# Optimization experiments

Measured on AMD Instinct MI355X. Metric: run time of the kernel, lower is better.

## Reference

```python
import jax, jax.numpy as jnp
import numpy as np

B, N, D = 1, 768, 256
H = 4
HD = D // H
K = 16
EDGE_DIM = 4
LN_EPS = 1e-5


def setup_inputs() -> dict:
    key = jax.random.key(0)
    ks = jax.random.split(key, 16)
    g = lambda k, shape, fan: jax.random.normal(k, shape, jnp.float32) / np.sqrt(fan)
    return {
        'x': jax.random.normal(ks[0], (B, N, D), jnp.float32),
        'Wqkv_w': g(ks[1], (D, 3 * D), D), 'Wqkv_b': jnp.zeros((3 * D,), jnp.float32),
        'out_w': g(ks[2], (D, D), D), 'out_b': jnp.zeros((D,), jnp.float32),
        'ffn1_w': g(ks[3], (2 * D, 2 * D), 2 * D), 'ffn1_b': jnp.zeros((2 * D,), jnp.float32),
        'ln_g': jnp.ones((2 * D,), jnp.float32), 'ln_b': jnp.zeros((2 * D,), jnp.float32),
        'ffn2_w': g(ks[4], (2 * D, D), 2 * D), 'ffn2_b': jnp.zeros((D,), jnp.float32),
        'e1_w': g(ks[5], (EDGE_DIM, 2 * H), EDGE_DIM), 'e1_b': jnp.zeros((2 * H,), jnp.float32),
        'e2_w': g(ks[6], (2 * H, H), 2 * H), 'e2_b': jnp.zeros((H,), jnp.float32),
        'graph_gate': jnp.float32(0.5),
    }


def _normalize(v):
    return v / jnp.clip(jnp.linalg.norm(v, axis=-1, keepdims=True), 1e-12)


def reference(x, Wqkv_w, Wqkv_b, out_w, out_b, ffn1_w, ffn1_b, ln_g, ln_b,
              ffn2_w, ffn2_b, e1_w, e1_b, e2_w, e2_b, graph_gate):
    b, n, d = x.shape
    # ---- graph topology (no grad, discrete top-k) ----
    xs = jax.lax.stop_gradient(x)
    dn_s = _normalize(xs)
    sim_d = jnp.einsum('bnd,bmd->bnm', dn_s, dn_s)
    eye = jnp.eye(n, dtype=bool)
    sim_d = jnp.where(eye, -jnp.inf, sim_d)
    idx = jax.lax.top_k(sim_d, K)[1]                       # (B,N,K)
    adj = jnp.zeros((b, n, n), bool).at[
        jnp.arange(b)[:, None, None], jnp.arange(n)[None, :, None], idx].set(True)
    adj = adj | jnp.swapaxes(adj, 1, 2) | eye              # symmetric + self loops
    # ---- differentiable edge features (B,N,N,4) ----
    dnm = _normalize(x)
    sim = jnp.einsum('bnd,bmd->bnm', dnm, dnm)
    diff = x[:, :, None, :] - x[:, None, :, :]             # (B,N,N,D) memory-bound
    l2 = jnp.linalg.norm(diff, axis=-1) / np.float32(np.sqrt(d))
    ad = jnp.abs(diff)
    ef = jnp.stack([sim, l2, ad.mean(-1), ad.max(-1)], axis=-1)
    # ---- edge bias per head (B,H,N,N) ----
    h = jax.nn.relu(ef @ e1_w + e1_b)
    bias = jnp.transpose(h @ e2_w + e2_b, (0, 3, 1, 2))
    # ---- attention ----
    qkv = (x @ Wqkv_w + Wqkv_b).reshape(b, n, H, HD, 3)
    qkv = jnp.transpose(qkv, (0, 2, 1, 3, 4))              # (B,H,N,HD,3)
    q, k, v = qkv[..., 0], qkv[..., 1], qkv[..., 2]
    logits = jnp.einsum('bhnd,bhmd->bhnm', q, k) / np.float32(np.sqrt(HD))
    logits = logits + graph_gate * bias
    logits = jnp.where(adj[:, None], logits, -jnp.inf)     # sparse masking
    attn = jax.nn.softmax(logits, axis=-1)
    ctx = jnp.einsum('bhnm,bhmd->bhnd', attn, v)
    msg = jnp.transpose(ctx, (0, 2, 1, 3)).reshape(b, n, d) @ out_w + out_b
    # ---- FFN: Linear -> LayerNorm -> GELU -> Linear, residual ----
    y = jnp.concatenate([x, msg], axis=-1) @ ffn1_w + ffn1_b
    mu = y.mean(-1, keepdims=True)
    var = ((y - mu) ** 2).mean(-1, keepdims=True)
    y = (y - mu) / jnp.sqrt(var + LN_EPS) * ln_g + ln_b
    y = jax.nn.gelu(y, approximate=False)
    return x + (y @ ffn2_w + ffn2_b)
```

## Files before the change

### kernel.cpp

```cpp
#include <hip/hip_runtime.h>
#include <hip/hip_bf16.h>
#include <math.h>

#define NN 768
#define DD 256
#define NHEAD 4
#define HDIM 64
#define TOPK 16

typedef __attribute__((ext_vector_type(8))) short short8;
typedef __attribute__((ext_vector_type(4))) float f32x4;

__device__ __forceinline__ unsigned short f2bf(float f) {
    unsigned u = __float_as_uint(f);
    unsigned r = u + 0x7fffu + ((u >> 16) & 1u);
    return (unsigned short)(r >> 16);
}

__global__ __launch_bounds__(64) void k_norms(const float* __restrict__ x,
                                              double* __restrict__ nrm2_d,
                                              double* __restrict__ nrm_d,
                                              double* __restrict__ invn_d,
                                              unsigned short* __restrict__ xb,
                                              unsigned int* __restrict__ adjw) {
    int n = blockIdx.x;
    int lane = threadIdx.x;
    int gid = n * 64 + lane;
    adjw[gid * 3 + 0] = 0u;
    adjw[gid * 3 + 1] = 0u;
    adjw[gid * 3 + 2] = 0u;
    const float* row = x + (size_t)n * DD;
    double s = 0.0;
    #pragma unroll
    for (int i = 0; i < 4; ++i) {
        float v = row[lane + 64 * i];
        xb[(size_t)n * DD + lane + 64 * i] = f2bf(v);
        s += (double)v * (double)v;
    }
    for (int off = 32; off > 0; off >>= 1) s += __shfl_down(s, off);
    if (lane == 0) {
        nrm2_d[n] = s;
        double nv = sqrt(s);
        nrm_d[n] = nv;
        invn_d[n] = 1.0 / fmax(nv, 1e-12);
    }
}

__global__ __launch_bounds__(256) void k_prep(const float* __restrict__ Wqkv,
                                              const float* __restrict__ outw,
                                              const float* __restrict__ f1w,
                                              const float* __restrict__ f2w,
                                              unsigned short* __restrict__ t_qkv,
                                              unsigned short* __restrict__ t_out,
                                              unsigned short* __restrict__ t_f1,
                                              unsigned short* __restrict__ t_f2) {
    int b = blockIdx.x;
    const float* src; unsigned short* dst; int K, C, tile;
    if (b < 192)      { src = Wqkv; dst = t_qkv; K = 256; C = 768; tile = b; }
    else if (b < 256) { src = outw; dst = t_out; K = 256; C = 256; tile = b - 192; }
    else if (b < 512) { src = f1w;  dst = t_f1;  K = 512; C = 512; tile = b - 256; }
    else              { src = f2w;  dst = t_f2;  K = 512; C = 256; tile = b - 512; }
    int tpr = C / 32;
    int k0 = (tile / tpr) * 32, c0 = (tile % tpr) * 32;
    __shared__ float tls[32][33];
    int tid = threadIdx.x;
    int r = tid >> 3, c4 = (tid & 7) * 4;
    float4 v = *(const float4*)&src[(size_t)(k0 + r) * C + c0 + c4];
    tls[r][c4 + 0] = v.x; tls[r][c4 + 1] = v.y;
    tls[r][c4 + 2] = v.z; tls[r][c4 + 3] = v.w;
    __syncthreads();
    int rc = tid >> 3, k4 = (tid & 7) * 4;
    unsigned short* d = &dst[(size_t)(c0 + rc) * K + k0 + k4];
    d[0] = f2bf(tls[k4 + 0][rc]);
    d[1] = f2bf(tls[k4 + 1][rc]);
    d[2] = f2bf(tls[k4 + 2][rc]);
    d[3] = f2bf(tls[k4 + 3][rc]);
}

__global__ __launch_bounds__(512) void k_sim(const float* __restrict__ x,
                                             const double* __restrict__ invn_d,
                                             double* __restrict__ simd) {
    int b = blockIdx.x;
    int r = (int)((sqrtf(8.f * (float)b + 1.f) - 1.f) * 0.5f);
    while ((r + 1) * (r + 2) / 2 <= b) ++r;
    while (r * (r + 1) / 2 > b) --r;
    int c = b - r * (r + 1) / 2;
    int n0 = c * 32, m0 = r * 32;

    int tid = threadIdx.x;
    int g = tid >> 8;
    int t = tid & 255;
    int tx = t & 15, ty = t >> 4;
    __shared__ float A[2][32][68];
    __shared__ float Bm[2][32][68];
    double d00 = 0.0, d01 = 0.0, d10 = 0.0, d11 = 0.0;

    #pragma unroll
    for (int kt = 0; kt < 2; ++kt) {
        int d0 = g * 128 + kt * 64;
        #pragma unroll
        for (int it = 0; it < 8; ++it) {
            int l = t + 256 * it;
            int rr = l >> 6, cc = l & 63;
            A[g][rr][cc]  = x[(size_t)(n0 + rr) * DD + d0 + cc];
            Bm[g][rr][cc] = x[(size_t)(m0 + rr) * DD + d0 + cc];
        }
        __syncthreads();
        for (int d = 0; d < 64; d += 4) {
            float4 b0 = *(const float4*)&Bm[g][tx][d];
            float4 b1 = *(const float4*)&Bm[g][tx + 16][d];
            float4 a0 = *(const float4*)&A[g][ty][d];
            float4 a1 = *(const float4*)&A[g][ty + 16][d];
            double b0x = b0.x, b0y = b0.y, b0z = b0.z, b0w = b0.w;
            double b1x = b1.x, b1y = b1.y, b1z = b1.z, b1w = b1.w;
            double a0x = a0.x, a0y = a0.y, a0z = a0.z, a0w = a0.w;
            double a1x = a1.x, a1y = a1.y, a1z = a1.z, a1w = a1.w;
            d00 += a0x * b0x + a0y * b0y + a0z * b0z + a0w * b0w;
            d01 += a0x * b1x + a0y * b1y + a0z * b1z + a0w * b1w;
            d10 += a1x * b0x + a1y * b0y + a1z * b0z + a1w * b0w;
            d11 += a1x * b1x + a1y * b1y + a1z * b1z + a1w * b1w;
        }
        __syncthreads();
    }

    double* part = (double*)&A[0][0][0];
    if (g == 1) {
        part[t * 4 + 0] = d00; part[t * 4 + 1] = d01;
        part[t * 4 + 2] = d10; part[t * 4 + 3] = d11;
    }
    __syncthreads();
    if (g == 0) {
        d00 += part[t * 4 + 0]; d01 += part[t * 4 + 1];
        d10 += part[t * 4 + 2]; d11 += part[t * 4 + 3];
        double in_m0 = invn_d[m0 + tx], in_m1 = invn_d[m0 + tx + 16];
        double in_n0 = invn_d[n0 + ty], in_n1 = invn_d[n0 + ty + 16];
        double v00 = d00 * in_n0 * in_m0;
        double v01 = d01 * in_n0 * in_m1;
        double v10 = d10 * in_n1 * in_m0;
        double v11 = d11 * in_n1 * in_m1;
        simd[(size_t)(n0 + ty) * NN + m0 + tx]           = v00;
        simd[(size_t)(n0 + ty) * NN + m0 + tx + 16]      = v01;
        simd[(size_t)(n0 + ty + 16) * NN + m0 + tx]      = v10;
        simd[(size_t)(n0 + ty + 16) * NN + m0 + tx + 16] = v11;
        simd[(size_t)(m0 + tx) * NN + n0 + ty]           = v00;
        simd[(size_t)(m0 + tx + 16) * NN + n0 + ty]      = v01;
        simd[(size_t)(m0 + tx) * NN + n0 + ty + 16]      = v10;
        simd[(size_t)(m0 + tx + 16) * NN + n0 + ty + 16] = v11;
    }
}

__global__ __launch_bounds__(256) void k_topk(const double* __restrict__ simd,
                                              unsigned char* __restrict__ adj) {
    int n = blockIdx.x;
    int tid = threadIdx.x;
    int w = tid >> 6, l = tid & 63;
    int mbase = w * 192 + l;
    const double* row = simd + (size_t)n * NN;
    double v0 = row[mbase];
    double v1 = row[mbase + 64];
    double v2 = row[mbase + 128];
    if (mbase == n)       v0 = -INFINITY;
    if (mbase + 64 == n)  v1 = -INFINITY;
    if (mbase + 128 == n) v2 = -INFINITY;
    if (tid == 0) adj[(size_t)n * NN + n] = 1;

    __shared__ double wv[2][4];
    __shared__ int    wi[2][4];

    for (int itr = 0; itr < TOPK; ++itr) {
        int p = itr & 1;
        double bv = v0; int bi = mbase;
        if (v1 > bv) { bv = v1; bi = mbase + 64; }
        if (v2 > bv) { bv = v2; bi = mbase + 128; }
        #pragma unroll
        for (int off = 32; off > 0; off >>= 1) {
            double ov = __shfl_down(bv, off);
            int    oi = __shfl_down(bi, off);
            if (ov > bv || (ov == bv && oi < bi)) { bv = ov; bi = oi; }
        }
        if (l == 0) { wv[p][w] = bv; wi[p][w] = bi; }
        __syncthreads();
        double fv = wv[p][0]; int fi = wi[p][0];
        #pragma unroll
        for (int ww = 1; ww < 4; ++ww) {
            double ov = wv[p][ww]; int oi = wi[p][ww];
            if (ov > fv || (ov == fv && oi < fi)) { fv = ov; fi = oi; }
        }
        if (fi == mbase)            v0 = -INFINITY;
        else if (fi == mbase + 64)  v1 = -INFINITY;
        else if (fi == mbase + 128) v2 = -INFINITY;
        if (tid == 0) {
            adj[(size_t)n * NN + fi] = 1;
            adj[(size_t)fi * NN + n] = 1;
        }
    }
}

__global__ __launch_bounds__(256) void k_edge_attn(
        const float* __restrict__ x,
        const double* __restrict__ nrm2_d,
        const double* __restrict__ nrm_d,
        const double* __restrict__ simd,
        const unsigned char* __restrict__ adj,
        const float* __restrict__ e1_w, const float* __restrict__ e1_b,
        const float* __restrict__ e2_w, const float* __restrict__ e2_b,
        const float* __restrict__ gate_p,
        const float* __restrict__ q, const float* __restrict__ k,
        const float* __restrict__ v,
        unsigned short* __restrict__ ctxb) {
    int n = blockIdx.x;
    int tid = threadIdx.x;
    int w = tid >> 6, l = tid & 63;
    __shared__ unsigned short idxs[NN];
    __shared__ float w_sh[NHEAD][NN];
    __shared__ float ef2s[NN];
    __shared__ float ef3s[NN];
    __shared__ float qsh[NHEAD][HDIM];
    __shared__ int wtot[4];

    int c = 0; int loc[3];
    #pragma unroll
    for (int i = 0; i < 3; ++i) {
        int m = 3 * tid + i;
        if (adj[(size_t)n * NN + m]) loc[c++] = m;
    }
    int pc = c;
    #pragma unroll
    for (int off = 1; off < 64; off <<= 1) {
        int o = __shfl_up(pc, off);
        if (l >= off) pc += o;
    }
    if (l == 63) wtot[w] = pc;
    qsh[w][l] = q[((size_t)w * NN + n) * HDIM + l];
    __syncthreads();
    int base = 0;
    #pragma unroll
    for (int ww = 0; ww < 4; ++ww) if (ww < w) base += wtot[ww];
    int start = base + pc - c;
    for (int i = 0; i < c; ++i) idxs[start + i] = (unsigned short)loc[i];
    int cnt = wtot[0] + wtot[1] + wtot[2] + wtot[3];
    __syncthreads();

    float xa[4];
    #pragma unroll
    for (int i = 0; i < 4; ++i) xa[i] = x[(size_t)n * DD + l + 64 * i];

    for (int j = w; j < cnt; j += 4) {
        int m = idxs[j];
        float sab = 0.f, mab = 0.f;
        #pragma unroll
        for (int i = 0; i < 4; ++i) {
            float xb = x[(size_t)m * DD + l + 64 * i];
            float ad = fabsf(xa[i] - xb);
            sab += ad;
            mab = fmaxf(mab, ad);
        }
        #pragma unroll
        for (int off = 32; off > 0; off >>= 1) {
            sab += __shfl_xor(sab, off);
            mab = fmaxf(mab, __shfl_xor(mab, off));
        }
        if (l == 0) { ef2s[j] = sab * (1.f / 256.f); ef3s[j] = mab; }
    }
    __syncthreads();

    double nrm2n = nrm2_d[n];
    double nrmn  = nrm_d[n];
    float gate = gate_p[0];
    for (int j0 = 0; j0 < cnt; j0 += 64) {
        int j = j0 + (tid >> 2);
        int hh = tid & 3;
        if (j < cnt) {
            int m = idxs[j];
            double s_d   = simd[(size_t)n * NN + m];
            double nrm2m = nrm2_d[m];
            double dotd  = s_d * nrmn * nrm_d[m];
            double l2sq  = fmax(nrm2n + nrm2m - 2.0 * dotd, 0.0);
            float ef0 = (float)s_d;
            float ef1 = (float)(sqrt(l2sq) * (1.0 / 16.0));
            float ef2 = ef2s[j];
            float ef3 = ef3s[j];
            float bb = e2_b[hh];
            #pragma unroll
            for (int jj = 0; jj < 8; ++jj) {
                float hv = e1_b[jj] + ef0 * e1_w[0 * 8 + jj] + ef1 * e1_w[1 * 8 + jj]
                         + ef2 * e1_w[2 * 8 + jj] + ef3 * e1_w[3 * 8 + jj];
                bb += fmaxf(hv, 0.f) * e2_w[jj * 4 + hh];
            }
            w_sh[hh][j] = gate * bb;
        }
    }
    __syncthreads();

    int h = w;
    float lmax = -INFINITY;
    for (int j = l; j < cnt; j += 64) {
        int m = idxs[j];
        const float4* kr = (const float4*)(k + ((size_t)h * NN + m) * HDIM);
        float dotv = 0.f;
        #pragma unroll
        for (int d4 = 0; d4 < HDIM / 4; ++d4) {
            float4 kv = kr[d4];
            dotv += qsh[h][4 * d4 + 0] * kv.x + qsh[h][4 * d4 + 1] * kv.y
                  + qsh[h][4 * d4 + 2] * kv.z + qsh[h][4 * d4 + 3] * kv.w;
        }
        w_sh[h][j] = dotv * 0.125f + w_sh[h][j];
        lmax = fmaxf(lmax, w_sh[h][j]);
    }
    #pragma unroll
    for (int off = 32; off > 0; off >>= 1)
        lmax = fmaxf(lmax, __shfl_xor(lmax, off));

    float lsum = 0.f;
    for (int j = l; j < cnt; j += 64) {
        float e = expf(w_sh[h][j] - lmax);
        w_sh[h][j] = e;
        lsum += e;
    }
    #pragma unroll
    for (int off = 32; off > 0; off >>= 1) lsum += __shfl_xor(lsum, off);
    float inv = 1.f / lsum;
    __syncthreads();

    float acc = 0.f;
    #pragma unroll 4
    for (int j = 0; j < cnt; ++j)
        acc += w_sh[h][j] * v[((size_t)h * NN + idxs[j]) * HDIM + l];
    ctxb[(size_t)n * DD + h * HDIM + l] = f2bf(acc * inv);
}

template<int KD, int MODE, bool CONCAT>
__global__ __launch_bounds__(256) void k_gemm_reg(const unsigned short* __restrict__ A,
                                                  const unsigned short* __restrict__ A2,
                                                  const unsigned short* __restrict__ Bt,
                                                  const float* __restrict__ bias,
                                                  const float* __restrict__ resid,
                                                  float* __restrict__ out,
                                                  unsigned short* __restrict__ outb,
                                                  float* __restrict__ q,
                                                  float* __restrict__ k,
                                                  float* __restrict__ v,
                                                  int ncols) {
    int tid = threadIdx.x;
    int w = tid >> 6, lane = tid & 63;
    int m0 = blockIdx.y * 64 + w * 16;
    int n0 = blockIdx.x * 16;
    int fr = lane & 15, fg = lane >> 4;
    f32x4 acc = {0.f, 0.f, 0.f, 0.f};

    const unsigned short* brow = &Bt[(size_t)(n0 + fr) * KD];
    #pragma unroll
    for (int k0 = 0; k0 < KD; k0 += 32) {
        const unsigned short* Asrc = A; int koff = k0;
        if (CONCAT && k0 >= 256) { Asrc = A2; koff = k0 - 256; }
        int lda = CONCAT ? 256 : KD;
        short8 a = *(const short8*)&Asrc[(size_t)(m0 + fr) * lda + koff + fg * 8];
        short8 b = *(const short8*)&brow[k0 + fg * 8];
        acc = __builtin_amdgcn_mfma_f32_16x16x32_bf16(a, b, acc, 0, 0, 0);
    }

    int cidx = n0 + fr;
    if (MODE == 2) {
        int hh = cidx / 192, rem = cidx % 192, hd = rem / 3, s = rem % 3;
        float* dst = (s == 0) ? q : (s == 1) ? k : v;
        float bb = bias[cidx];
        #pragma unroll
        for (int r = 0; r < 4; ++r) {
            int n = m0 + fg * 4 + r;
            dst[((size_t)hh * NN + n) * HDIM + hd] = acc[r] + bb;
        }
    } else {
        float bb = bias[cidx];
        #pragma unroll
        for (int r = 0; r < 4; ++r) {
            int n = m0 + fg * 4 + r;
            float val = acc[r] + bb;
            if (MODE == 1) val += resid[(size_t)n * ncols + cidx];
            if (MODE == 3) outb[(size_t)n * ncols + cidx] = f2bf(val);
            else           out [(size_t)n * ncols + cidx] = val;
        }
    }
}

__global__ __launch_bounds__(256) void k_ln_gelu(const float* __restrict__ y,
                                                 const float* __restrict__ g,
                                                 const float* __restrict__ b,
                                                 unsigned short* __restrict__ ybb) {
    int n = blockIdx.x;
    int tid = threadIdx.x;
    const float* row = y + (size_t)n * 512;
    __shared__ float red[256];
    float v0 = row[tid], v1 = row[tid + 256];

    red[tid] = v0 + v1; __syncthreads();
    for (int s = 128; s > 0; s >>= 1) {
        if (tid < s) red[tid] += red[tid + s];
        __syncthreads();
    }
    float mu = red[0] * (1.f / 512.f);
    __syncthreads();

    float d0 = v0 - mu, d1 = v1 - mu;
    red[tid] = d0 * d0 + d1 * d1; __syncthreads();
    for (int s = 128; s > 0; s >>= 1) {
        if (tid < s) red[tid] += red[tid + s];
        __syncthreads();
    }
    float var = red[0] * (1.f / 512.f);
    float rstd = 1.f / sqrtf(var + 1e-5f);

    float z0 = d0 * rstd * g[tid] + b[tid];
    float z1 = d1 * rstd * g[tid + 256] + b[tid + 256];
    float o0 = 0.5f * z0 * (1.f + erff(z0 * 0.70710678118654752f));
    float o1 = 0.5f * z1 * (1.f + erff(z1 * 0.70710678118654752f));
    ybb[(size_t)n * 512 + tid]       = f2bf(o0);
    ybb[(size_t)n * 512 + tid + 256] = f2bf(o1);
}

extern "C" void kernel_launch(void* const* d_in, const int* in_sizes, int n_in,
                              void* d_out, int out_size, void* d_ws, size_t ws_size,
                              hipStream_t stream) {
    const float* x       = (const float*)d_in[0];
    const float* Wqkv_w  = (const float*)d_in[1];
    const float* Wqkv_b  = (const float*)d_in[2];
    const float* out_w   = (const float*)d_in[3];
    const float* out_b   = (const float*)d_in[4];
    const float* ffn1_w  = (const float*)d_in[5];
    const float* ffn1_b  = (const float*)d_in[6];
    const float* ln_g    = (const float*)d_in[7];
    const float* ln_b    = (const float*)d_in[8];
    const float* ffn2_w  = (const float*)d_in[9];
    const float* ffn2_b  = (const float*)d_in[10];
    const float* e1_w    = (const float*)d_in[11];
    const float* e1_b    = (const float*)d_in[12];
    const float* e2_w    = (const float*)d_in[13];
    const float* e2_b    = (const float*)d_in[14];
    const float* gate    = (const float*)d_in[15];

    char* base = (char*)d_ws;
    double* simd   = (double*)base;            base += (size_t)NN * NN * 8;
    double* nrm2_d = (double*)base;            base += NN * 8;
    double* nrm_d  = (double*)base;            base += NN * 8;
    double* invn_d = (double*)base;            base += NN * 8;
    float* qb      = (float*)base;             base += (size_t)NN * DD * 4;
    float* kb      = (float*)base;             base += (size_t)NN * DD * 4;
    float* vb      = (float*)base;             base += (size_t)NN * DD * 4;
    float* yb      = (float*)base;             base += (size_t)NN * 512 * 4;
    unsigned char* adj = (unsigned char*)base;  base += (size_t)NN * NN;
    unsigned short* xbf  = (unsigned short*)base; base += (size_t)NN * DD * 2;
    unsigned short* ctxb = (unsigned short*)base; base += (size_t)NN * DD * 2;
    unsigned short* msgb = (unsigned short*)base; base += (size_t)NN * DD * 2;
    unsigned short* ybb  = (unsigned short*)base; base += (size_t)NN * 512 * 2;
    unsigned short* t_qkv = (unsigned short*)base; base += (size_t)768 * 256 * 2;
    unsigned short* t_out = (unsigned short*)base; base += (size_t)256 * 256 * 2;
    unsigned short* t_f1  = (unsigned short*)base; base += (size_t)512 * 512 * 2;
    unsigned short* t_f2  = (unsigned short*)base; base += (size_t)256 * 512 * 2;

    k_prep<<<640, 256, 0, stream>>>(Wqkv_w, out_w, ffn1_w, ffn2_w,
                                    t_qkv, t_out, t_f1, t_f2);

    k_norms<<<NN, 64, 0, stream>>>(x, nrm2_d, nrm_d, invn_d, xbf,
                                   (unsigned int*)adj);

    k_sim<<<24 * 25 / 2, 512, 0, stream>>>(x, invn_d, simd);

    k_gemm_reg<DD, 2, false><<<dim3(48, 12), 256, 0, stream>>>(
        xbf, nullptr, t_qkv, Wqkv_b, nullptr, nullptr, nullptr, qb, kb, vb, 3 * DD);

    k_topk<<<NN, 256, 0, stream>>>(simd, adj);

    k_edge_attn<<<NN, 256, 0, stream>>>(x, nrm2_d, nrm_d, simd, adj,
                                        e1_w, e1_b, e2_w, e2_b, gate,
                                        qb, kb, vb, ctxb);

    k_gemm_reg<DD, 3, false><<<dim3(16, 12), 256, 0, stream>>>(
        ctxb, nullptr, t_out, out_b, nullptr, nullptr, msgb, nullptr, nullptr, nullptr, DD);

    k_gemm_reg<512, 0, true><<<dim3(32, 12), 256, 0, stream>>>(
        xbf, msgb, t_f1, ffn1_b, nullptr, yb, nullptr, nullptr, nullptr, nullptr, 512);

    k_ln_gelu<<<NN, 256, 0, stream>>>(yb, ln_g, ln_b, ybb);

    k_gemm_reg<512, 1, false><<<dim3(16, 12), 256, 0, stream>>>(
        ybb, nullptr, t_f2, ffn2_b, x, (float*)d_out, nullptr, nullptr, nullptr, nullptr, DD);
}
```

Before: 88.23 us.

## Merge prep/norms, sim/QKV kernels and fuse tail into cooperative kernel

Merges the weight-transpose and norm kernels into one launch, runs the similarity GEMM and QKV projection as disjoint block ranges of a single kernel, and replaces the four tail launches (out-proj, FFN1, LayerNorm+GELU, FFN2) with one cooperative kernel that separates the phases with grid syncs. The aim is to cut per-launch overhead and the idle gaps between short dependent kernels. In exchange it adds grid-wide barriers and runs the tail on only 256 blocks, and the QKV blocks still read t_qkv from the previous launch.

```diff
diff --git a/kernel.cpp b/kernel.cpp
--- a/kernel.cpp
+++ b/kernel.cpp
@@ -1,6 +1,9 @@
 #include <hip/hip_runtime.h>
 #include <hip/hip_bf16.h>
+#include <hip/hip_cooperative_groups.h>
 #include <math.h>
+
+namespace cg = cooperative_groups;
 
 #define NN 768
 #define DD 256
@@ -17,135 +20,161 @@
     return (unsigned short)(r >> 16);
 }
 
-__global__ __launch_bounds__(64) void k_norms(const float* __restrict__ x,
-                                              double* __restrict__ nrm2_d,
-                                              double* __restrict__ nrm_d,
-                                              double* __restrict__ invn_d,
-                                              unsigned short* __restrict__ xb,
-                                              unsigned int* __restrict__ adjw) {
-    int n = blockIdx.x;
-    int lane = threadIdx.x;
-    int gid = n * 64 + lane;
-    adjw[gid * 3 + 0] = 0u;
-    adjw[gid * 3 + 1] = 0u;
-    adjw[gid * 3 + 2] = 0u;
-    const float* row = x + (size_t)n * DD;
-    double s = 0.0;
-    #pragma unroll
-    for (int i = 0; i < 4; ++i) {
-        float v = row[lane + 64 * i];
-        xb[(size_t)n * DD + lane + 64 * i] = f2bf(v);
-        s += (double)v * (double)v;
-    }
-    for (int off = 32; off > 0; off >>= 1) s += __shfl_down(s, off);
-    if (lane == 0) {
-        nrm2_d[n] = s;
-        double nv = sqrt(s);
-        nrm_d[n] = nv;
-        invn_d[n] = 1.0 / fmax(nv, 1e-12);
-    }
-}
-
-__global__ __launch_bounds__(256) void k_prep(const float* __restrict__ Wqkv,
-                                              const float* __restrict__ outw,
-                                              const float* __restrict__ f1w,
-                                              const float* __restrict__ f2w,
-                                              unsigned short* __restrict__ t_qkv,
-                                              unsigned short* __restrict__ t_out,
-                                              unsigned short* __restrict__ t_f1,
-                                              unsigned short* __restrict__ t_f2) {
+__global__ __launch_bounds__(256) void k_prep_norms(
+        const float* __restrict__ Wqkv, const float* __restrict__ outw,
+        const float* __restrict__ f1w,  const float* __restrict__ f2w,
+        unsigned short* __restrict__ t_qkv, unsigned short* __restrict__ t_out,
+        unsigned short* __restrict__ t_f1,  unsigned short* __restrict__ t_f2,
+        const float* __restrict__ x,
+        double* __restrict__ nrm2_d, double* __restrict__ nrm_d,
+        double* __restrict__ invn_d,
+        unsigned short* __restrict__ xb, unsigned int* __restrict__ adjw) {
     int b = blockIdx.x;
-    const float* src; unsigned short* dst; int K, C, tile;
-    if (b < 192)      { src = Wqkv; dst = t_qkv; K = 256; C = 768; tile = b; }
-    else if (b < 256) { src = outw; dst = t_out; K = 256; C = 256; tile = b - 192; }
-    else if (b < 512) { src = f1w;  dst = t_f1;  K = 512; C = 512; tile = b - 256; }
-    else              { src = f2w;  dst = t_f2;  K = 512; C = 256; tile = b - 512; }
-    int tpr = C / 32;
-    int k0 = (tile / tpr) * 32, c0 = (tile % tpr) * 32;
-    __shared__ float tls[32][33];
     int tid = threadIdx.x;
-    int r = tid >> 3, c4 = (tid & 7) * 4;
-    float4 v = *(const float4*)&src[(size_t)(k0 + r) * C + c0 + c4];
-    tls[r][c4 + 0] = v.x; tls[r][c4 + 1] = v.y;
-    tls[r][c4 + 2] = v.z; tls[r][c4 + 3] = v.w;
-    __syncthreads();
-    int rc = tid >> 3, k4 = (tid & 7) * 4;
-    unsigned short* d = &dst[(size_t)(c0 + rc) * K + k0 + k4];
-    d[0] = f2bf(tls[k4 + 0][rc]);
-    d[1] = f2bf(tls[k4 + 1][rc]);
-    d[2] = f2bf(tls[k4 + 2][rc]);
-    d[3] = f2bf(tls[k4 + 3][rc]);
-}
-
-__global__ __launch_bounds__(512) void k_sim(const float* __restrict__ x,
-                                             const double* __restrict__ invn_d,
-                                             double* __restrict__ simd) {
-    int b = blockIdx.x;
-    int r = (int)((sqrtf(8.f * (float)b + 1.f) - 1.f) * 0.5f);
-    while ((r + 1) * (r + 2) / 2 <= b) ++r;
-    while (r * (r + 1) / 2 > b) --r;
-    int c = b - r * (r + 1) / 2;
-    int n0 = c * 32, m0 = r * 32;
-
-    int tid = threadIdx.x;
-    int g = tid >> 8;
-    int t = tid & 255;
-    int tx = t & 15, ty = t >> 4;
+    if (b < 640) {
+        const float* src; unsigned short* dst; int K, C, tile;
+        if (b < 192)      { src = Wqkv; dst = t_qkv; K = 256; C = 768; tile = b; }
+        else if (b < 256) { src = outw; dst = t_out; K = 256; C = 256; tile = b - 192; }
+        else if (b < 512) { src = f1w;  dst = t_f1;  K = 512; C = 512; tile = b - 256; }
+        else              { src = f2w;  dst = t_f2;  K = 512; C = 256; tile = b - 512; }
+        int tpr = C / 32;
+        int k0 = (tile / tpr) * 32, c0 = (tile % tpr) * 32;
+        __shared__ float tls[32][33];
+        int r = tid >> 3, c4 = (tid & 7) * 4;
+        float4 v = *(const float4*)&src[(size_t)(k0 + r) * C + c0 + c4];
+        tls[r][c4 + 0] = v.x; tls[r][c4 + 1] = v.y;
+        tls[r][c4 + 2] = v.z; tls[r][c4 + 3] = v.w;
+        __syncthreads();
+        int rc = tid >> 3, k4 = (tid & 7) * 4;
+        unsigned short* d = &dst[(size_t)(c0 + rc) * K + k0 + k4];
+        d[0] = f2bf(tls[k4 + 0][rc]);
+        d[1] = f2bf(tls[k4 + 1][rc]);
+        d[2] = f2bf(tls[k4 + 2][rc]);
+        d[3] = f2bf(tls[k4 + 3][rc]);
+    } else {
+        int nb = b - 640;
+        int gid = nb * 256 + tid;
+        adjw[gid * 3 + 0] = 0u;
+        adjw[gid * 3 + 1] = 0u;
+        adjw[gid * 3 + 2] = 0u;
+        int n = nb * 4 + (tid >> 6);
+        int lane = tid & 63;
+        const float* row = x + (size_t)n * DD;
+        double s = 0.0;
+        #pragma unroll
+        for (int i = 0; i < 4; ++i) {
+            float v = row[lane + 64 * i];
+            xb[(size_t)n * DD + lane + 64 * i] = f2bf(v);
+            s += (double)v * (double)v;
+        }
+        for (int off = 32; off > 0; off >>= 1) s += __shfl_down(s, off);
+        if (lane == 0) {
+            nrm2_d[n] = s;
+            double nv = sqrt(s);
+            nrm_d[n] = nv;
+            invn_d[n] = 1.0 / fmax(nv, 1e-12);
+        }
+    }
+}
+
+__global__ __launch_bounds__(512) void k_simqkv(
+        const float* __restrict__ x, const double* __restrict__ invn_d,
+        double* __restrict__ simd,
+        const unsigned short* __restrict__ xbf,
+        const unsigned short* __restrict__ t_qkv,
+        const float* __restrict__ Wqkv_b,
+        float* __restrict__ qb, float* __restrict__ kb, float* __restrict__ vb) {
     __shared__ float A[2][32][68];
     __shared__ float Bm[2][32][68];
-    double d00 = 0.0, d01 = 0.0, d10 = 0.0, d11 = 0.0;
-
-    #pragma unroll
-    for (int kt = 0; kt < 2; ++kt) {
-        int d0 = g * 128 + kt * 64;
-        #pragma unroll
-        for (int it = 0; it < 8; ++it) {
-            int l = t + 256 * it;
-            int rr = l >> 6, cc = l & 63;
-            A[g][rr][cc]  = x[(size_t)(n0 + rr) * DD + d0 + cc];
-            Bm[g][rr][cc] = x[(size_t)(m0 + rr) * DD + d0 + cc];
+    int b = blockIdx.x;
+    int tid = threadIdx.x;
+    if (b < 300) {
+        int r = (int)((sqrtf(8.f * (float)b + 1.f) - 1.f) * 0.5f);
+        while ((r + 1) * (r + 2) / 2 <= b) ++r;
+        while (r * (r + 1) / 2 > b) --r;
+        int c = b - r * (r + 1) / 2;
+        int n0 = c * 32, m0 = r * 32;
+
+        int g = tid >> 8;
+        int t = tid & 255;
+        int tx = t & 15, ty = t >> 4;
+        double d00 = 0.0, d01 = 0.0, d10 = 0.0, d11 = 0.0;
+
+        #pragma unroll
+        for (int kt = 0; kt < 2; ++kt) {
+            int d0 = g * 128 + kt * 64;
+            #pragma unroll
+            for (int it = 0; it < 8; ++it) {
+                int l = t + 256 * it;
+                int rr = l >> 6, cc = l & 63;
+                A[g][rr][cc]  = x[(size_t)(n0 + rr) * DD + d0 + cc];
+                Bm[g][rr][cc] = x[(size_t)(m0 + rr) * DD + d0 + cc];
+            }
+            __syncthreads();
+            for (int d = 0; d < 64; d += 4) {
+                float4 b0 = *(const float4*)&Bm[g][tx][d];
+                float4 b1 = *(const float4*)&Bm[g][tx + 16][d];
+                float4 a0 = *(const float4*)&A[g][ty][d];
+                float4 a1 = *(const float4*)&A[g][ty + 16][d];
+                double b0x = b0.x, b0y = b0.y, b0z = b0.z, b0w = b0.w;
+                double b1x = b1.x, b1y = b1.y, b1z = b1.z, b1w = b1.w;
+                double a0x = a0.x, a0y = a0.y, a0z = a0.z, a0w = a0.w;
+                double a1x = a1.x, a1y = a1.y, a1z = a1.z, a1w = a1.w;
+                d00 += a0x * b0x + a0y * b0y + a0z * b0z + a0w * b0w;
+                d01 += a0x * b1x + a0y * b1y + a0z * b1z + a0w * b1w;
+                d10 += a1x * b0x + a1y * b0y + a1z * b0z + a1w * b0w;
+                d11 += a1x * b1x + a1y * b1y + a1z * b1z + a1w * b1w;
+            }
+            __syncthreads();
+        }
+
+        double* part = (double*)&A[0][0][0];
+        if (g == 1) {
+            part[t * 4 + 0] = d00; part[t * 4 + 1] = d01;
+            part[t * 4 + 2] = d10; part[t * 4 + 3] = d11;
         }
         __syncthreads();
-        for (int d = 0; d < 64; d += 4) {
-            float4 b0 = *(const float4*)&Bm[g][tx][d];
-            float4 b1 = *(const float4*)&Bm[g][tx + 16][d];
-            float4 a0 = *(const float4*)&A[g][ty][d];
-            float4 a1 = *(const float4*)&A[g][ty + 16][d];
-            double b0x = b0.x, b0y = b0.y, b0z = b0.z, b0w = b0.w;
-            double b1x = b1.x, b1y = b1.y, b1z = b1.z, b1w = b1.w;
-            double a0x = a0.x, a0y = a0.y, a0z = a0.z, a0w = a0.w;
-            double a1x = a1.x, a1y = a1.y, a1z = a1.z, a1w = a1.w;
-            d00 += a0x * b0x + a0y * b0y + a0z * b0z + a0w * b0w;
-            d01 += a0x * b1x + a0y * b1y + a0z * b1z + a0w * b1w;
-            d10 += a1x * b0x + a1y * b0y + a1z * b0z + a1w * b0w;
-            d11 += a1x * b1x + a1y * b1y + a1z * b1z + a1w * b1w;
-        }
-        __syncthreads();
-    }
-
-    double* part = (double*)&A[0][0][0];
-    if (g == 1) {
-        part[t * 4 + 0] = d00; part[t * 4 + 1] = d01;
-        part[t * 4 + 2] = d10; part[t * 4 + 3] = d11;
-    }
-    __syncthreads();
-    if (g == 0) {
-        d00 += part[t * 4 + 0]; d01 += part[t * 4 + 1];
-        d10 += part[t * 4 + 2]; d11 += part[t * 4 + 3];
-        double in_m0 = invn_d[m0 + tx], in_m1 = invn_d[m0 + tx + 16];
-        double in_n0 = invn_d[n0 + ty], in_n1 = invn_d[n0 + ty + 16];
-        double v00 = d00 * in_n0 * in_m0;
-        double v01 = d01 * in_n0 * in_m1;
-        double v10 = d10 * in_n1 * in_m0;
-        double v11 = d11 * in_n1 * in_m1;
-        simd[(size_t)(n0 + ty) * NN + m0 + tx]           = v00;
-        simd[(size_t)(n0 + ty) * NN + m0 + tx + 16]      = v01;
-        simd[(size_t)(n0 + ty + 16) * NN + m0 + tx]      = v10;
-        simd[(size_t)(n0 + ty + 16) * NN + m0 + tx + 16] = v11;
-        simd[(size_t)(m0 + tx) * NN + n0 + ty]           = v00;
-        simd[(size_t)(m0 + tx + 16) * NN + n0 + ty]      = v01;
-        simd[(size_t)(m0 + tx) * NN + n0 + ty + 16]      = v10;
-        simd[(size_t)(m0 + tx + 16) * NN + n0 + ty + 16] = v11;
+        if (g == 0) {
+            d00 += part[t * 4 + 0]; d01 += part[t * 4 + 1];
+            d10 += part[t * 4 + 2]; d11 += part[t * 4 + 3];
+            double in_m0 = invn_d[m0 + tx], in_m1 = invn_d[m0 + tx + 16];
+            double in_n0 = invn_d[n0 + ty], in_n1 = invn_d[n0 + ty + 16];
+            double v00 = d00 * in_n0 * in_m0;
+            double v01 = d01 * in_n0 * in_m1;
+            double v10 = d10 * in_n1 * in_m0;
+            double v11 = d11 * in_n1 * in_m1;
+            simd[(size_t)(n0 + ty) * NN + m0 + tx]           = v00;
+            simd[(size_t)(n0 + ty) * NN + m0 + tx + 16]      = v01;
+            simd[(size_t)(n0 + ty + 16) * NN + m0 + tx]      = v10;
+            simd[(size_t)(n0 + ty + 16) * NN + m0 + tx + 16] = v11;
+            simd[(size_t)(m0 + tx) * NN + n0 + ty]           = v00;
+            simd[(size_t)(m0 + tx + 16) * NN + n0 + ty]      = v01;
+            simd[(size_t)(m0 + tx) * NN + n0 + ty + 16]      = v10;
+            simd[(size_t)(m0 + tx + 16) * NN + n0 + ty + 16] = v11;
+        }
+    } else {
+        int w = tid >> 6, lane = tid & 63;
+        int id = (b - 300) * 8 + w;
+        int rt = id % 48, ct = id / 48;
+        int m0 = rt * 16, n0 = ct * 16;
+        int fr = lane & 15, fg = lane >> 4;
+        f32x4 acc = {0.f, 0.f, 0.f, 0.f};
+        const unsigned short* brow = &t_qkv[(size_t)(n0 + fr) * DD];
+        #pragma unroll
+        for (int k0 = 0; k0 < DD; k0 += 32) {
+            short8 a = *(const short8*)&xbf[(size_t)(m0 + fr) * DD + k0 + fg * 8];
+            short8 bb8 = *(const short8*)&brow[k0 + fg * 8];
+            acc = __builtin_amdgcn_mfma_f32_16x16x32_bf16(a, bb8, acc, 0, 0, 0);
+        }
+        int cidx = n0 + fr;
+        int hh = cidx / 192, rem = cidx % 192, hd = rem / 3, s = rem % 3;
+        float* dst = (s == 0) ? qb : (s == 1) ? kb : vb;
+        float bb = Wqkv_b[cidx];
+        #pragma unroll
+        for (int r = 0; r < 4; ++r) {
+            int n = m0 + fg * 4 + r;
+            dst[((size_t)hh * NN + n) * HDIM + hd] = acc[r] + bb;
+        }
     }
 }
 
@@ -329,92 +358,108 @@
     ctxb[(size_t)n * DD + h * HDIM + l] = f2bf(acc * inv);
 }
 
-template<int KD, int MODE, bool CONCAT>
-__global__ __launch_bounds__(256) void k_gemm_reg(const unsigned short* __restrict__ A,
-                                                  const unsigned short* __restrict__ A2,
-                                                  const unsigned short* __restrict__ Bt,
-                                                  const float* __restrict__ bias,
-                                                  const float* __restrict__ resid,
-                                                  float* __restrict__ out,
-                                                  unsigned short* __restrict__ outb,
-                                                  float* __restrict__ q,
-                                                  float* __restrict__ k,
-                                                  float* __restrict__ v,
-                                                  int ncols) {
+__global__ __launch_bounds__(256) void k_tail(
+        const unsigned short* __restrict__ ctxb,
+        const unsigned short* __restrict__ t_out, const float* __restrict__ out_b,
+        const unsigned short* __restrict__ xbf,
+        unsigned short* __restrict__ msgb,
+        const unsigned short* __restrict__ t_f1, const float* __restrict__ ffn1_b,
+        float* __restrict__ yb,
+        const float* __restrict__ ln_g, const float* __restrict__ ln_b,
+        unsigned short* __restrict__ ybb,
+        const unsigned short* __restrict__ t_f2, const float* __restrict__ ffn2_b,
+        const float* __restrict__ x, float* __restrict__ outp) {
+    cg::grid_group grid = cg::this_grid();
     int tid = threadIdx.x;
     int w = tid >> 6, lane = tid & 63;
-    int m0 = blockIdx.y * 64 + w * 16;
-    int n0 = blockIdx.x * 16;
+    int g = blockIdx.x * 4 + w;
     int fr = lane & 15, fg = lane >> 4;
-    f32x4 acc = {0.f, 0.f, 0.f, 0.f};
-
-    const unsigned short* brow = &Bt[(size_t)(n0 + fr) * KD];
-    #pragma unroll
-    for (int k0 = 0; k0 < KD; k0 += 32) {
-        const unsigned short* Asrc = A; int koff = k0;
-        if (CONCAT && k0 >= 256) { Asrc = A2; koff = k0 - 256; }
-        int lda = CONCAT ? 256 : KD;
-        short8 a = *(const short8*)&Asrc[(size_t)(m0 + fr) * lda + koff + fg * 8];
-        short8 b = *(const short8*)&brow[k0 + fg * 8];
-        acc = __builtin_amdgcn_mfma_f32_16x16x32_bf16(a, b, acc, 0, 0, 0);
-    }
-
-    int cidx = n0 + fr;
-    if (MODE == 2) {
-        int hh = cidx / 192, rem = cidx % 192, hd = rem / 3, s = rem % 3;
-        float* dst = (s == 0) ? q : (s == 1) ? k : v;
-        float bb = bias[cidx];
+
+    if (g < 768) {
+        int rt = g % 48, ct = g / 48;
+        int m0 = rt * 16, n0 = ct * 16;
+        f32x4 acc = {0.f, 0.f, 0.f, 0.f};
+        const unsigned short* brow = &t_out[(size_t)(n0 + fr) * DD];
+        #pragma unroll
+        for (int k0 = 0; k0 < DD; k0 += 32) {
+            short8 a = *(const short8*)&ctxb[(size_t)(m0 + fr) * DD + k0 + fg * 8];
+            short8 b = *(const short8*)&brow[k0 + fg * 8];
+            acc = __builtin_amdgcn_mfma_f32_16x16x32_bf16(a, b, acc, 0, 0, 0);
+        }
+        float bb = out_b[n0 + fr];
+        #pragma unroll
+        for (int r = 0; r < 4; ++r)
+            msgb[(size_t)(m0 + fg * 4 + r) * DD + n0 + fr] = f2bf(acc[r] + bb);
+    }
+    __threadfence();
+    grid.sync();
+
+    for (int t = g; t < 1536; t += 1024) {
+        int rt = t % 48, ct = t / 48;
+        int m0 = rt * 16, n0 = ct * 16;
+        f32x4 acc = {0.f, 0.f, 0.f, 0.f};
+        const unsigned short* brow = &t_f1[(size_t)(n0 + fr) * 512];
+        #pragma unroll
+        for (int k0 = 0; k0 < 512; k0 += 32) {
+            const unsigned short* Asrc = (k0 < 256) ? xbf : msgb;
+            int koff = (k0 < 256) ? k0 : k0 - 256;
+            short8 a = *(const short8*)&Asrc[(size_t)(m0 + fr) * DD + koff + fg * 8];
+            short8 b = *(const short8*)&brow[k0 + fg * 8];
+            acc = __builtin_amdgcn_mfma_f32_16x16x32_bf16(a, b, acc, 0, 0, 0);
+        }
+        float bb = ffn1_b[n0 + fr];
+        #pragma unroll
+        for (int r = 0; r < 4; ++r)
+            yb[(size_t)(m0 + fg * 4 + r) * 512 + n0 + fr] = acc[r] + bb;
+    }
+    __threadfence();
+    grid.sync();
+
+    if (g < 768) {
+        const float* row = yb + (size_t)g * 512;
+        float vv[8];
+        float s = 0.f;
+        #pragma unroll
+        for (int i = 0; i < 8; ++i) { vv[i] = row[lane + 64 * i]; s += vv[i]; }
+        #pragma unroll
+        for (int off = 32; off > 0; off >>= 1) s += __shfl_xor(s, off);
+        float mu = s * (1.f / 512.f);
+        float qs = 0.f;
+        #pragma unroll
+        for (int i = 0; i < 8; ++i) { float d = vv[i] - mu; qs += d * d; }
+        #pragma unroll
+        for (int off = 32; off > 0; off >>= 1) qs += __shfl_xor(qs, off);
+        float rstd = 1.f / sqrtf(qs * (1.f / 512.f) + 1e-5f);
+        #pragma unroll
+        for (int i = 0; i < 8; ++i) {
+            int cidx = lane + 64 * i;
+            float z = (vv[i] - mu) * rstd * ln_g[cidx] + ln_b[cidx];
+            float o = 0.5f * z * (1.f + erff(z * 0.70710678118654752f));
+            ybb[(size_t)g * 512 + cidx] = f2bf(o);
+        }
+    }
+    __threadfence();
+    grid.sync();
+
+    if (g < 768) {
+        int rt = g % 48, ct = g / 48;
+        int m0 = rt * 16, n0 = ct * 16;
+        f32x4 acc = {0.f, 0.f, 0.f, 0.f};
+        const unsigned short* brow = &t_f2[(size_t)(n0 + fr) * 512];
+        #pragma unroll
+        for (int k0 = 0; k0 < 512; k0 += 32) {
+            short8 a = *(const short8*)&ybb[(size_t)(m0 + fr) * 512 + k0 + fg * 8];
+            short8 b = *(const short8*)&brow[k0 + fg * 8];
+            acc = __builtin_amdgcn_mfma_f32_16x16x32_bf16(a, b, acc, 0, 0, 0);
+        }
+        float bb = ffn2_b[n0 + fr];
         #pragma unroll
         for (int r = 0; r < 4; ++r) {
             int n = m0 + fg * 4 + r;
-            dst[((size_t)hh * NN + n) * HDIM + hd] = acc[r] + bb;
-        }
-    } else {
-        float bb = bias[cidx];
-        #pragma unroll
-        for (int r = 0; r < 4; ++r) {
-            int n = m0 + fg * 4 + r;
-            float val = acc[r] + bb;
-            if (MODE == 1) val += resid[(size_t)n * ncols + cidx];
-            if (MODE == 3) outb[(size_t)n * ncols + cidx] = f2bf(val);
-            else           out [(size_t)n * ncols + cidx] = val;
-        }
-    }
-}
-
-__global__ __launch_bounds__(256) void k_ln_gelu(const float* __restrict__ y,
-                                                 const float* __restrict__ g,
-                                                 const float* __restrict__ b,
-                                                 unsigned short* __restrict__ ybb) {
-    int n = blockIdx.x;
-    int tid = threadIdx.x;
-    const float* row = y + (size_t)n * 512;
-    __shared__ float red[256];
-    float v0 = row[tid], v1 = row[tid + 256];
-
-    red[tid] = v0 + v1; __syncthreads();
-    for (int s = 128; s > 0; s >>= 1) {
-        if (tid < s) red[tid] += red[tid + s];
-        __syncthreads();
-    }
-    float mu = red[0] * (1.f / 512.f);
-    __syncthreads();
-
-    float d0 = v0 - mu, d1 = v1 - mu;
-    red[tid] = d0 * d0 + d1 * d1; __syncthreads();
-    for (int s = 128; s > 0; s >>= 1) {
-        if (tid < s) red[tid] += red[tid + s];
-        __syncthreads();
-    }
-    float var = red[0] * (1.f / 512.f);
-    float rstd = 1.f / sqrtf(var + 1e-5f);
-
-    float z0 = d0 * rstd * g[tid] + b[tid];
-    float z1 = d1 * rstd * g[tid + 256] + b[tid + 256];
-    float o0 = 0.5f * z0 * (1.f + erff(z0 * 0.70710678118654752f));
-    float o1 = 0.5f * z1 * (1.f + erff(z1 * 0.70710678118654752f));
-    ybb[(size_t)n * 512 + tid]       = f2bf(o0);
-    ybb[(size_t)n * 512 + tid + 256] = f2bf(o1);
+            outp[(size_t)n * DD + n0 + fr] =
+                acc[r] + bb + x[(size_t)n * DD + n0 + fr];
+        }
+    }
 }
 
 extern "C" void kernel_launch(void* const* d_in, const int* in_sizes, int n_in,
@@ -455,17 +500,15 @@
     unsigned short* t_out = (unsigned short*)base; base += (size_t)256 * 256 * 2;
     unsigned short* t_f1  = (unsigned short*)base; base += (size_t)512 * 512 * 2;
     unsigned short* t_f2  = (unsigned short*)base; base += (size_t)256 * 512 * 2;
-
-    k_prep<<<640, 256, 0, stream>>>(Wqkv_w, out_w, ffn1_w, ffn2_w,
-                                    t_qkv, t_out, t_f1, t_f2);
-
-    k_norms<<<NN, 64, 0, stream>>>(x, nrm2_d, nrm_d, invn_d, xbf,
-                                   (unsigned int*)adj);
-
-    k_sim<<<24 * 25 / 2, 512, 0, stream>>>(x, invn_d, simd);
-
-    k_gemm_reg<DD, 2, false><<<dim3(48, 12), 256, 0, stream>>>(
-        xbf, nullptr, t_qkv, Wqkv_b, nullptr, nullptr, nullptr, qb, kb, vb, 3 * DD);
+    float* outp = (float*)d_out;
+
+    k_prep_norms<<<832, 256, 0, stream>>>(Wqkv_w, out_w, ffn1_w, ffn2_w,
+                                          t_qkv, t_out, t_f1, t_f2,
+                                          x, nrm2_d, nrm_d, invn_d, xbf,
+                                          (unsigned int*)adj);
+
+    k_simqkv<<<588, 512, 0, stream>>>(x, invn_d, simd, xbf, t_qkv, Wqkv_b,
+                                      qb, kb, vb);
 
     k_topk<<<NN, 256, 0, stream>>>(simd, adj);
 
@@ -473,14 +516,12 @@
                                         e1_w, e1_b, e2_w, e2_b, gate,
                                         qb, kb, vb, ctxb);
 
-    k_gemm_reg<DD, 3, false><<<dim3(16, 12), 256, 0, stream>>>(
-        ctxb, nullptr, t_out, out_b, nullptr, nullptr, msgb, nullptr, nullptr, nullptr, DD);
-
-    k_gemm_reg<512, 0, true><<<dim3(32, 12), 256, 0, stream>>>(
-        xbf, msgb, t_f1, ffn1_b, nullptr, yb, nullptr, nullptr, nullptr, nullptr, 512);
-
-    k_ln_gelu<<<NN, 256, 0, stream>>>(yb, ln_g, ln_b, ybb);
-
-    k_gemm_reg<512, 1, false><<<dim3(16, 12), 256, 0, stream>>>(
-        ybb, nullptr, t_f2, ffn2_b, x, (float*)d_out, nullptr, nullptr, nullptr, nullptr, DD);
-}
+    void* args[] = { (void*)&ctxb, (void*)&t_out, (void*)&out_b,
+                     (void*)&xbf, (void*)&msgb,
+                     (void*)&t_f1, (void*)&ffn1_b, (void*)&yb,
+                     (void*)&ln_g, (void*)&ln_b, (void*)&ybb,
+                     (void*)&t_f2, (void*)&ffn2_b,
+                     (void*)&x, (void*)&outp };
+    hipLaunchCooperativeKernel(reinterpret_cast<void*>(k_tail),
+                               dim3(256), dim3(256), args, 0, stream);
+}
```

Result: slower. 231.4 us (+162.3%).
